# Kernel tuning notes

Measured on AMD Instinct MI355X. Metric: run time of the kernel, lower is better.

Reference implementation:

```python
import jax, jax.numpy as jnp
import numpy as np

T_SYN = 201
SYN_BASIS_NO = 3


def setup_inputs() -> dict:
    key = jax.random.key(0)
    ks = jax.random.split(key, 5)
    T_data, n_e, n_i, sub_no, B = 100000, 500, 200, 20, SYN_BASIS_NO
    S_e = jax.random.uniform(ks[0], (T_data, n_e), jnp.float32)
    S_i = jax.random.uniform(ks[1], (T_data, n_i), jnp.float32)
    C_syn_e = jax.random.uniform(ks[2], (sub_no, n_e), jnp.float32)
    C_syn_i = jax.random.uniform(ks[3], (sub_no, n_i), jnp.float32)
    # init values from the torch module
    K_syn = jnp.concatenate([jnp.full((sub_no, B, 1), 0.02, jnp.float32),
                             jnp.full((sub_no, B, 1), -0.02, jnp.float32)], axis=-1)
    tau_syn = jnp.tile(jnp.arange(1.6, 1.6 + B, dtype=jnp.float32).reshape(-1, 1), (1, 2))
    delta_syn = 2.0 * jax.random.uniform(ks[4], (sub_no, 2), jnp.float32)
    return dict(S_e=S_e, S_i=S_i, C_syn_e=C_syn_e, C_syn_i=C_syn_i,
                K_syn=K_syn, tau_syn=tau_syn, delta_syn=delta_syn)


def _kernels(K_syn, tau_syn, delta_syn):
    # Vectorized alpha-function kernel bank: [sub_no, 2(e/i), T_syn]
    t = jnp.arange(T_SYN, dtype=jnp.float32)                     # [T]
    ts = t[None, None, :] - delta_syn[:, :, None]                # [S,2,T]
    ts = jnp.where(ts < 0.0, 0.0, ts)                            # clamp like t[t<0]=0
    tau = jnp.exp(tau_syn)                                       # [B,2]
    tt = ts[:, None, :, :] / tau[None, :, :, None]               # [S,B,2,T]
    basis = tt * jnp.exp(-tt)                                    # alpha functions
    return jnp.einsum('sbct,sbc->sct', basis, K_syn)             # [S,2,T]


def _causal_conv(x, kern):
    # x: [T_data, S]; kern: [S, T_syn]; out[t,s] = sum_k kern[s,k] * x[t-k,s]
    S = x.shape[1]
    lhs = x.T[None]                          # [1,S,T_data]
    rhs = kern[:, ::-1][:, None, :]          # flip -> lax correlation == causal conv
    out = jax.lax.conv_general_dilated(lhs, rhs, (1,), [(T_SYN - 1, 0)],
                                       feature_group_count=S,
                                       dimension_numbers=('NCH', 'OIH', 'NCH'))
    return out[0].T                          # [T_data, S]


def reference(S_e, S_i, C_syn_e, C_syn_i, K_syn, tau_syn, delta_syn):
    kern = _kernels(K_syn, tau_syn, delta_syn)   # [S,2,T_syn]
    in_e = S_e @ C_syn_e.T                       # [T_data, sub_no]
    in_i = S_i @ C_syn_i.T                       # [T_data, sub_no]
    return _causal_conv(in_e, kern[:, 0]) + _causal_conv(in_i, kern[:, 1])
```

## Files before the change

kernel.cpp:

```cpp
#include <hip/hip_runtime.h>
#include <hip/hip_bf16.h>

#define TDATA 100000
#define NE 500
#define NI 200
#define SUB 20
#define NB 3
#define TSYN 201

#define SROW 100552
#define HROW 216
#define STEPS_E 32
#define STEPS_I 13
#define FULL_E 31
#define FULL_I 12
#define GEMM_BLKS 782

#define OFF_HP  0
#define OFF_BE  8640
#define OFF_BI  (OFF_BE + 8192)
#define OFF_INT (OFF_BI + 3328)

typedef __bf16 bf16x8 __attribute__((ext_vector_type(8)));
typedef float  f32x16 __attribute__((ext_vector_type(16)));

__global__ __launch_bounds__(256) void setup_kernel(
    const float* __restrict__ C_e, const float* __restrict__ C_i,
    const float* __restrict__ K_syn, const float* __restrict__ tau_syn,
    const float* __restrict__ delta_syn, float* __restrict__ ws)
{
    int idx = blockIdx.x * 256 + threadIdx.x;
    if (idx < 8640) {
        int c = idx / (SUB * HROW);
        int rem = idx - c * (SUB * HROW);
        int s = rem / HROW;
        int k = (rem - s * HROW) - 8;
        float v = 0.f;
        if (k >= 0 && k < TSYN) {
            float ts = (float)k - delta_syn[s * 2 + c];
            ts = ts < 0.f ? 0.f : ts;
            #pragma unroll
            for (int b = 0; b < NB; b++) {
                float tt = ts / expf(tau_syn[b * 2 + c]);
                v += K_syn[(s * NB + b) * 2 + c] * tt * expf(-tt);
            }
        }
        ws[OFF_HP + idx] = v;
    } else if (idx < 30720) {
        int j = idx - 8640;
        const int PERROW = 552;
        int row = j / PERROW;
        int e = j - row * PERROW;
        int off = (e < 200) ? e : (200 + TDATA + (e - 200));
        ws[OFF_INT + (long)row * SROW + off] = 0.f;
    } else if (idx < 47104) {
        int j = idx - 30720;
        int step = j >> 9;
        int lane = (j >> 3) & 63;
        int jj = j & 7;
        int k = step * 16 + ((lane >> 5) << 3) + jj;
        int s = lane & 31;
        float v = (s < SUB && k < NE) ? C_e[s * NE + k] : 0.f;
        ((__hip_bfloat16*)(ws + OFF_BE))[j] = (__hip_bfloat16)v;
    } else {
        int j = idx - 47104;
        int step = j >> 9;
        int lane = (j >> 3) & 63;
        int jj = j & 7;
        int k = step * 16 + ((lane >> 5) << 3) + jj;
        int s = lane & 31;
        float v = (s < SUB && k < NI) ? C_i[s * NI + k] : 0.f;
        ((__hip_bfloat16*)(ws + OFF_BI))[j] = (__hip_bfloat16)v;
    }
}

template<int K, int FULL>
__device__ __forceinline__ void gemm_body(
    const float* __restrict__ S, const float* __restrict__ wsA,
    float* __restrict__ inT, long row0, int lane)
{
    const int n = lane & 31, h = lane >> 5;
    long row = row0 + n; if (row >= TDATA) row = TDATA - 1;
    const float* rp = S + row * (long)K + h * 8;
    const bf16x8* afr = (const bf16x8*)wsA;
    f32x16 acc = {};

    #pragma unroll 4
    for (int u = 0; u < FULL; u++) {
        float4 lo = *(const float4*)(rp + 16 * u);
        float4 hi = *(const float4*)(rp + 16 * u + 4);
        bf16x8 b;
        b[0] = (__bf16)lo.x; b[1] = (__bf16)lo.y; b[2] = (__bf16)lo.z; b[3] = (__bf16)lo.w;
        b[4] = (__bf16)hi.x; b[5] = (__bf16)hi.y; b[6] = (__bf16)hi.z; b[7] = (__bf16)hi.w;
        bf16x8 a = afr[u * 64 + lane];
        acc = __builtin_amdgcn_mfma_f32_32x32x16_bf16(a, b, acc, 0, 0, 0);
    }
    {
        int kb = FULL * 16 + h * 8;
        float4 lo = make_float4(0.f, 0.f, 0.f, 0.f);
        float4 hi = make_float4(0.f, 0.f, 0.f, 0.f);
        if (kb + 8 <= K) {
            lo = *(const float4*)(rp + 16 * FULL);
            hi = *(const float4*)(rp + 16 * FULL + 4);
        } else if (kb + 4 <= K) {
            lo = *(const float4*)(rp + 16 * FULL);
        }
        bf16x8 b;
        b[0] = (__bf16)lo.x; b[1] = (__bf16)lo.y; b[2] = (__bf16)lo.z; b[3] = (__bf16)lo.w;
        b[4] = (__bf16)hi.x; b[5] = (__bf16)hi.y; b[6] = (__bf16)hi.z; b[7] = (__bf16)hi.w;
        bf16x8 a = afr[FULL * 64 + lane];
        acc = __builtin_amdgcn_mfma_f32_32x32x16_bf16(a, b, acc, 0, 0, 0);
    }

    long t = row0 + n;
    #pragma unroll
    for (int r = 0; r < 16; r++) {
        int m = (r & 3) + 8 * (r >> 2) + 4 * h;
        if (m < SUB && t < TDATA)
            inT[(long)m * SROW + 200 + t] = acc[r];
    }
}

__global__ __launch_bounds__(256) void gemm_kernel(
    const float* __restrict__ Se, const float* __restrict__ Si,
    float* __restrict__ ws)
{
    int lane = threadIdx.x & 63, wave = threadIdx.x >> 6;
    if (blockIdx.x < GEMM_BLKS) {
        long row0 = (long)blockIdx.x * 128 + wave * 32;
        gemm_body<NE, FULL_E>(Se, ws + OFF_BE, ws + OFF_INT, row0, lane);
    } else {
        long row0 = (long)(blockIdx.x - GEMM_BLKS) * 128 + wave * 32;
        gemm_body<NI, FULL_I>(Si, ws + OFF_BI,
                              ws + OFF_INT + (long)SUB * SROW, row0, lane);
    }
}

#define SW(i) ((i) + ((i) >> 5))

__global__ __launch_bounds__(256) void conv_kernel(
    const float* __restrict__ ws, float* __restrict__ out)
{
    __shared__ __align__(16) float W[2][2336];
    __shared__ __align__(16) float HT[2][208];
    const int tid = threadIdx.x;
    const int s = blockIdx.y;
    const long t0 = (long)blockIdx.x * 2048;

    for (int i = tid; i < 1128; i += 256) {
        int c = i >= 564;
        int i4 = i - c * 564;
        float4 v = *(const float4*)(ws + OFF_INT + (long)(c * SUB + s) * SROW
                                    + t0 - 8 + 4 * i4);
        int b = 4 * i4;
        int p = SW(b);
        W[c][p] = v.x; W[c][p + 1] = v.y; W[c][p + 2] = v.z; W[c][p + 3] = v.w;
    }
    if (tid < 104) {
        int c = tid >= 52;
        int j4 = (tid - c * 52) * 4;
        *(float4*)&HT[c][j4] =
            *(const float4*)(ws + OFF_HP + (c * SUB + s) * HROW + 8 + j4);
    }
    __syncthreads();

    float acc[8];
    #pragma unroll
    for (int r = 0; r < 8; r++) acc[r] = 0.f;

    #pragma unroll
    for (int c = 0; c < 2; c++) {
        #pragma unroll 2
        for (int g = 0; g < 26; g++) {
            int k0 = g << 3;
            int xb = (tid << 3) + 200 - k0;
            float x[16];
            #pragma unroll
            for (int q = 0; q < 16; q++) x[q] = W[c][SW(xb + q)];
            float h[8];
            *(float4*)&h[0] = *(const float4*)&HT[c][k0];
            *(float4*)&h[4] = *(const float4*)&HT[c][k0 + 4];
            #pragma unroll
            for (int j = 0; j < 8; j++)
                #pragma unroll
                for (int r = 0; r < 8; r++)
                    acc[r] += h[j] * x[8 + r - j];
        }
    }

    #pragma unroll
    for (int r = 0; r < 8; r++) {
        long t = t0 + 8 * tid + r;
        if (t < TDATA) out[t * SUB + s] = acc[r];
    }
}

extern "C" void kernel_launch(void* const* d_in, const int* in_sizes, int n_in,
                              void* d_out, int out_size, void* d_ws, size_t ws_size,
                              hipStream_t stream)
{
    const float* S_e     = (const float*)d_in[0];
    const float* S_i     = (const float*)d_in[1];
    const float* C_e     = (const float*)d_in[2];
    const float* C_i     = (const float*)d_in[3];
    const float* K_syn   = (const float*)d_in[4];
    const float* tau_syn = (const float*)d_in[5];
    const float* delta   = (const float*)d_in[6];
    float* out = (float*)d_out;
    float* ws  = (float*)d_ws;

    hipLaunchKernelGGL(setup_kernel, dim3(210), dim3(256), 0, stream,
                       C_e, C_i, K_syn, tau_syn, delta, ws);
    hipLaunchKernelGGL(gemm_kernel, dim3(2 * GEMM_BLKS), dim3(256), 0, stream,
                       S_e, S_i, ws);
    hipLaunchKernelGGL(conv_kernel, dim3(49, SUB), dim3(256), 0, stream,
                       ws, out);
}
```

Measured before the change: 405.7 us.

## Stage GEMM input tiles in LDS via direct global-to-LDS loads with split-K waves

Each block now copies a contiguous 32-row tile of S into shared memory with global_load_lds, so the global reads are fully coalesced instead of strided per-row float4 loads. The four waves then split the K dimension of the MFMA loop and combine their partial accumulators through LDS before wave 0 writes the result. This replaces poorly coalesced HBM access with one bulk copy, at the cost of 64 KB of LDS per block (lower occupancy), a synchronous wait with no overlap, and extra reduction traffic.

Measured after the change: 400.2 us. Within noise of the previous version (-1.3%).

```diff
diff --git a/kernel.cpp b/kernel.cpp
--- a/kernel.cpp
+++ b/kernel.cpp
@@ -12,9 +12,7 @@
 #define HROW 216
 #define STEPS_E 32
 #define STEPS_I 13
-#define FULL_E 31
-#define FULL_I 12
-#define GEMM_BLKS 782
+#define NTILE 3125
 
 #define OFF_HP  0
 #define OFF_BE  8640
@@ -74,50 +72,72 @@
     }
 }
 
-template<int K, int FULL>
-__device__ __forceinline__ void gemm_body(
+template<int K, int STEPS>
+__device__ __forceinline__ void gemm2_body(
     const float* __restrict__ S, const float* __restrict__ wsA,
-    float* __restrict__ inT, long row0, int lane)
-{
+    float* __restrict__ inT, float* tile, int blk, int tid)
+{
+    const long gb = (long)blk * (32 * K);
+    constexpr int TB = 32 * K * 4;
+    {
+        auto gsrc = (const __attribute__((address_space(1))) char*)(const void*)(S + gb);
+        auto ldst = (__attribute__((address_space(3))) char*)(void*)tile;
+        for (int off = tid * 16; off < TB; off += 4096)
+            __builtin_amdgcn_global_load_lds(gsrc + off, ldst + off, 16, 0, 0);
+    }
+    asm volatile("s_waitcnt vmcnt(0)" ::: "memory");
+    __syncthreads();
+
+    const int lane = tid & 63, wave = tid >> 6;
     const int n = lane & 31, h = lane >> 5;
-    long row = row0 + n; if (row >= TDATA) row = TDATA - 1;
-    const float* rp = S + row * (long)K + h * 8;
+    const float* rp = tile + n * K;
     const bf16x8* afr = (const bf16x8*)wsA;
     f32x16 acc = {};
 
     #pragma unroll 4
-    for (int u = 0; u < FULL; u++) {
-        float4 lo = *(const float4*)(rp + 16 * u);
-        float4 hi = *(const float4*)(rp + 16 * u + 4);
+    for (int u = wave; u < STEPS; u += 4) {
+        const int kb = u * 16 + h * 8;
+        float4 lo = make_float4(0.f, 0.f, 0.f, 0.f);
+        float4 hi = make_float4(0.f, 0.f, 0.f, 0.f);
+        if (kb + 8 <= K) {
+            lo = *(const float4*)(rp + kb);
+            hi = *(const float4*)(rp + kb + 4);
+        } else if (kb + 4 <= K) {
+            lo = *(const float4*)(rp + kb);
+        }
         bf16x8 b;
         b[0] = (__bf16)lo.x; b[1] = (__bf16)lo.y; b[2] = (__bf16)lo.z; b[3] = (__bf16)lo.w;
         b[4] = (__bf16)hi.x; b[5] = (__bf16)hi.y; b[6] = (__bf16)hi.z; b[7] = (__bf16)hi.w;
         bf16x8 a = afr[u * 64 + lane];
         acc = __builtin_amdgcn_mfma_f32_32x32x16_bf16(a, b, acc, 0, 0, 0);
     }
-    {
-        int kb = FULL * 16 + h * 8;
-        float4 lo = make_float4(0.f, 0.f, 0.f, 0.f);
-        float4 hi = make_float4(0.f, 0.f, 0.f, 0.f);
-        if (kb + 8 <= K) {
-            lo = *(const float4*)(rp + 16 * FULL);
-            hi = *(const float4*)(rp + 16 * FULL + 4);
-        } else if (kb + 4 <= K) {
-            lo = *(const float4*)(rp + 16 * FULL);
-        }
-        bf16x8 b;
-        b[0] = (__bf16)lo.x; b[1] = (__bf16)lo.y; b[2] = (__bf16)lo.z; b[3] = (__bf16)lo.w;
-        b[4] = (__bf16)hi.x; b[5] = (__bf16)hi.y; b[6] = (__bf16)hi.z; b[7] = (__bf16)hi.w;
-        bf16x8 a = afr[FULL * 64 + lane];
-        acc = __builtin_amdgcn_mfma_f32_32x32x16_bf16(a, b, acc, 0, 0, 0);
-    }
-
-    long t = row0 + n;
-    #pragma unroll
-    for (int r = 0; r < 16; r++) {
-        int m = (r & 3) + 8 * (r >> 2) + 4 * h;
-        if (m < SUB && t < TDATA)
-            inT[(long)m * SROW + 200 + t] = acc[r];
+
+    __syncthreads();
+    if (wave != 0) {
+        float4* dst = (float4*)(tile + ((wave - 1) * 64 + lane) * 16);
+        dst[0] = make_float4(acc[0],  acc[1],  acc[2],  acc[3]);
+        dst[1] = make_float4(acc[4],  acc[5],  acc[6],  acc[7]);
+        dst[2] = make_float4(acc[8],  acc[9],  acc[10], acc[11]);
+        dst[3] = make_float4(acc[12], acc[13], acc[14], acc[15]);
+    }
+    __syncthreads();
+    if (wave == 0) {
+        #pragma unroll
+        for (int w = 0; w < 3; w++) {
+            const float4* src = (const float4*)(tile + (w * 64 + lane) * 16);
+            float4 p0 = src[0], p1 = src[1], p2 = src[2], p3 = src[3];
+            acc[0]  += p0.x; acc[1]  += p0.y; acc[2]  += p0.z; acc[3]  += p0.w;
+            acc[4]  += p1.x; acc[5]  += p1.y; acc[6]  += p1.z; acc[7]  += p1.w;
+            acc[8]  += p2.x; acc[9]  += p2.y; acc[10] += p2.z; acc[11] += p2.w;
+            acc[12] += p3.x; acc[13] += p3.y; acc[14] += p3.z; acc[15] += p3.w;
+        }
+        const long t = (long)blk * 32 + n;
+        #pragma unroll
+        for (int r = 0; r < 16; r++) {
+            int m = (r & 3) + 8 * (r >> 2) + 4 * h;
+            if (m < SUB)
+                inT[(long)m * SROW + 200 + t] = acc[r];
+        }
     }
 }
 
@@ -125,15 +145,14 @@
     const float* __restrict__ Se, const float* __restrict__ Si,
     float* __restrict__ ws)
 {
-    int lane = threadIdx.x & 63, wave = threadIdx.x >> 6;
-    if (blockIdx.x < GEMM_BLKS) {
-        long row0 = (long)blockIdx.x * 128 + wave * 32;
-        gemm_body<NE, FULL_E>(Se, ws + OFF_BE, ws + OFF_INT, row0, lane);
-    } else {
-        long row0 = (long)(blockIdx.x - GEMM_BLKS) * 128 + wave * 32;
-        gemm_body<NI, FULL_I>(Si, ws + OFF_BI,
-                              ws + OFF_INT + (long)SUB * SROW, row0, lane);
-    }
+    __shared__ float tile[32 * NE];
+    const int tid = threadIdx.x;
+    if (blockIdx.x < NTILE)
+        gemm2_body<NE, STEPS_E>(Se, ws + OFF_BE, ws + OFF_INT,
+                                tile, blockIdx.x, tid);
+    else
+        gemm2_body<NI, STEPS_I>(Si, ws + OFF_BI, ws + OFF_INT + (long)SUB * SROW,
+                                tile, blockIdx.x - NTILE, tid);
 }
 
 #define SW(i) ((i) + ((i) >> 5))
@@ -211,7 +230,7 @@
 
     hipLaunchKernelGGL(setup_kernel, dim3(210), dim3(256), 0, stream,
                        C_e, C_i, K_syn, tau_syn, delta, ws);
-    hipLaunchKernelGGL(gemm_kernel, dim3(2 * GEMM_BLKS), dim3(256), 0, stream,
+    hipLaunchKernelGGL(gemm_kernel, dim3(2 * NTILE), dim3(256), 0, stream,
                        S_e, S_i, ws);
     hipLaunchKernelGGL(conv_kernel, dim3(49, SUB), dim3(256), 0, stream,
                        ws, out);
```

## Stream GEMM input through LDS with async double-buffered loads and reuse conv registers

Applied to the files above, without the earlier changes.

The GEMM now stages S rows into per-wave LDS buffers with global_load_lds, double-buffering 32-column chunks so loads overlap MFMA work. It also preloads the A fragments into registers and uses an XOR swizzle to avoid bank conflicts. The conv kernel switches to vectorized float4 LDS reads with a sliding register window that reuses the previous group's data instead of reloading 16 scalars per group. The aim is to hide global memory latency in the memory-bound GEMM, at the cost of more registers and reliance on manual vmcnt waits. Setup grid and padding sizes change to match the new chunk layout.

After: 1.196 ms. 195% more time.

```diff
diff --git a/kernel.cpp b/kernel.cpp
--- a/kernel.cpp
+++ b/kernel.cpp
@@ -10,16 +10,14 @@
 
 #define SROW 100552
 #define HROW 216
-#define STEPS_E 32
-#define STEPS_I 13
-#define FULL_E 31
-#define FULL_I 12
-#define GEMM_BLKS 782
+#define NC_E 16
+#define NC_I 7
+#define NBLK 782
 
 #define OFF_HP  0
 #define OFF_BE  8640
 #define OFF_BI  (OFF_BE + 8192)
-#define OFF_INT (OFF_BI + 3328)
+#define OFF_INT (OFF_BI + 3584)
 
 typedef __bf16 bf16x8 __attribute__((ext_vector_type(8)));
 typedef float  f32x16 __attribute__((ext_vector_type(16)));
@@ -74,49 +72,78 @@
     }
 }
 
-template<int K, int FULL>
-__device__ __forceinline__ void gemm_body(
+template<int K>
+__device__ __forceinline__ void issue_chunk(
+    const float* __restrict__ S, const float* __restrict__ zrp,
+    long row0, int c, float* buf, int rsel, int slotl)
+{
+    #pragma unroll
+    for (int q = 0; q < 4; q++) {
+        const int kg = c * 32 + slotl;
+        const float* src = (kg + 4 <= K)
+            ? (S + (row0 + 8 * q + rsel) * (long)K + kg) : zrp;
+        __builtin_amdgcn_global_load_lds(
+            (const __attribute__((address_space(1))) char*)(const void*)src,
+            (__attribute__((address_space(3))) char*)(void*)(buf + q * 256),
+            16, 0, 0);
+    }
+}
+
+template<int K, int NC>
+__device__ __forceinline__ void gemm3_body(
     const float* __restrict__ S, const float* __restrict__ wsA,
-    float* __restrict__ inT, long row0, int lane)
-{
+    float* __restrict__ inT, const float* __restrict__ zrp,
+    float* buf0, float* buf1, long tile, int lane)
+{
+    constexpr int NSTEP = 2 * NC;
+    const long row0 = tile * 32;
     const int n = lane & 31, h = lane >> 5;
-    long row = row0 + n; if (row >= TDATA) row = TDATA - 1;
-    const float* rp = S + row * (long)K + h * 8;
+    const int rsel = lane >> 3;
+    const int slotl = 4 * ((lane & 7) ^ rsel);
+    const int xr = (n & 7) << 2;
+
     const bf16x8* afr = (const bf16x8*)wsA;
+    bf16x8 A[NSTEP];
+    #pragma unroll
+    for (int u = 0; u < NSTEP; u++) A[u] = afr[u * 64 + lane];
+
+    issue_chunk<K>(S, zrp, row0, 0, buf0, rsel, slotl);
+    issue_chunk<K>(S, zrp, row0, 1, buf1, rsel, slotl);
+
     f32x16 acc = {};
-
-    #pragma unroll 4
-    for (int u = 0; u < FULL; u++) {
-        float4 lo = *(const float4*)(rp + 16 * u);
-        float4 hi = *(const float4*)(rp + 16 * u + 4);
-        bf16x8 b;
-        b[0] = (__bf16)lo.x; b[1] = (__bf16)lo.y; b[2] = (__bf16)lo.z; b[3] = (__bf16)lo.w;
-        b[4] = (__bf16)hi.x; b[5] = (__bf16)hi.y; b[6] = (__bf16)hi.z; b[7] = (__bf16)hi.w;
-        bf16x8 a = afr[u * 64 + lane];
-        acc = __builtin_amdgcn_mfma_f32_32x32x16_bf16(a, b, acc, 0, 0, 0);
-    }
-    {
-        int kb = FULL * 16 + h * 8;
-        float4 lo = make_float4(0.f, 0.f, 0.f, 0.f);
-        float4 hi = make_float4(0.f, 0.f, 0.f, 0.f);
-        if (kb + 8 <= K) {
-            lo = *(const float4*)(rp + 16 * FULL);
-            hi = *(const float4*)(rp + 16 * FULL + 4);
-        } else if (kb + 4 <= K) {
-            lo = *(const float4*)(rp + 16 * FULL);
+    #pragma unroll
+    for (int c = 0; c < NC; c++) {
+        if (c < NC - 1) asm volatile("s_waitcnt vmcnt(4)" ::: "memory");
+        else            asm volatile("s_waitcnt vmcnt(0)" ::: "memory");
+        __builtin_amdgcn_sched_barrier(0);
+
+        float* buf = (c & 1) ? buf1 : buf0;
+        const float* r0 = buf + n * 32;
+        bf16x8 bf[2];
+        #pragma unroll
+        for (int uu = 0; uu < 2; uu++) {
+            const int kl = 16 * uu + 8 * h;
+            float4 lo = *(const float4*)(r0 + (kl ^ xr));
+            float4 hi = *(const float4*)(r0 + ((kl + 4) ^ xr));
+            bf16x8 b;
+            b[0] = (__bf16)lo.x; b[1] = (__bf16)lo.y; b[2] = (__bf16)lo.z; b[3] = (__bf16)lo.w;
+            b[4] = (__bf16)hi.x; b[5] = (__bf16)hi.y; b[6] = (__bf16)hi.z; b[7] = (__bf16)hi.w;
+            bf[uu] = b;
         }
-        bf16x8 b;
-        b[0] = (__bf16)lo.x; b[1] = (__bf16)lo.y; b[2] = (__bf16)lo.z; b[3] = (__bf16)lo.w;
-        b[4] = (__bf16)hi.x; b[5] = (__bf16)hi.y; b[6] = (__bf16)hi.z; b[7] = (__bf16)hi.w;
-        bf16x8 a = afr[FULL * 64 + lane];
-        acc = __builtin_amdgcn_mfma_f32_32x32x16_bf16(a, b, acc, 0, 0, 0);
-    }
-
-    long t = row0 + n;
+        __builtin_amdgcn_sched_barrier(0);
+        if (c + 2 < NC)
+            issue_chunk<K>(S, zrp, row0, c + 2, buf, rsel, slotl);
+        #pragma unroll
+        for (int uu = 0; uu < 2; uu++)
+            acc = __builtin_amdgcn_mfma_f32_32x32x16_bf16(A[2 * c + uu], bf[uu],
+                                                          acc, 0, 0, 0);
+    }
+
+    const long t = row0 + n;
     #pragma unroll
     for (int r = 0; r < 16; r++) {
         int m = (r & 3) + 8 * (r >> 2) + 4 * h;
-        if (m < SUB && t < TDATA)
+        if (m < SUB)
             inT[(long)m * SROW + 200 + t] = acc[r];
     }
 }
@@ -125,66 +152,83 @@
     const float* __restrict__ Se, const float* __restrict__ Si,
     float* __restrict__ ws)
 {
-    int lane = threadIdx.x & 63, wave = threadIdx.x >> 6;
-    if (blockIdx.x < GEMM_BLKS) {
-        long row0 = (long)blockIdx.x * 128 + wave * 32;
-        gemm_body<NE, FULL_E>(Se, ws + OFF_BE, ws + OFF_INT, row0, lane);
+    __shared__ float lds[4][2][1024];
+    const int lane = threadIdx.x & 63, wave = threadIdx.x >> 6;
+    if (blockIdx.x < NBLK) {
+        long tile = (long)blockIdx.x * 4 + wave;
+        if (tile >= 3125) return;
+        gemm3_body<NE, NC_E>(Se, ws + OFF_BE, ws + OFF_INT, ws + OFF_INT,
+                             lds[wave][0], lds[wave][1], tile, lane);
     } else {
-        long row0 = (long)(blockIdx.x - GEMM_BLKS) * 128 + wave * 32;
-        gemm_body<NI, FULL_I>(Si, ws + OFF_BI,
-                              ws + OFF_INT + (long)SUB * SROW, row0, lane);
-    }
-}
-
-#define SW(i) ((i) + ((i) >> 5))
+        long tile = (long)(blockIdx.x - NBLK) * 4 + wave;
+        if (tile >= 3125) return;
+        gemm3_body<NI, NC_I>(Si, ws + OFF_BI, ws + OFF_INT + (long)SUB * SROW,
+                             ws + OFF_INT, lds[wave][0], lds[wave][1], tile, lane);
+    }
+}
+
+#define SW(i) ((i) + (((i) >> 5) << 2))
+
+#define CONV_G(G, LO, HI, DOLOAD) {                                        \
+    float4 h0 = *(const float4*)&HT[c][8 * (G)];                           \
+    float4 h1 = *(const float4*)&HT[c][8 * (G) + 4];                       \
+    float hv[8] = {h0.x, h0.y, h0.z, h0.w, h1.x, h1.y, h1.z, h1.w};        \
+    _Pragma("unroll")                                                      \
+    for (int j = 0; j < 8; j++) {                                          \
+        _Pragma("unroll")                                                  \
+        for (int r = 0; r < 8; r++) {                                      \
+            const int ix = 8 + r - j;                                      \
+            acc[r] += hv[j] * ((ix < 8) ? LO[ix] : HI[ix - 8]);            \
+        }                                                                  \
+    }                                                                      \
+    if (DOLOAD) {                                                          \
+        const int a0 = wb + 216 - 8 * (G);                                 \
+        *(float4*)&LO[0] = *(const float4*)&W[c][SW(a0)];                  \
+        *(float4*)&LO[4] = *(const float4*)&W[c][SW(a0 + 4)];              \
+    }                                                                      \
+}
 
 __global__ __launch_bounds__(256) void conv_kernel(
     const float* __restrict__ ws, float* __restrict__ out)
 {
-    __shared__ __align__(16) float W[2][2336];
+    __shared__ __align__(16) float W[2][2560];
     __shared__ __align__(16) float HT[2][208];
     const int tid = threadIdx.x;
     const int s = blockIdx.y;
     const long t0 = (long)blockIdx.x * 2048;
 
     for (int i = tid; i < 1128; i += 256) {
-        int c = i >= 564;
-        int i4 = i - c * 564;
-        float4 v = *(const float4*)(ws + OFF_INT + (long)(c * SUB + s) * SROW
+        int cch = i >= 564;
+        int i4 = i - cch * 564;
+        float4 v = *(const float4*)(ws + OFF_INT + (long)(cch * SUB + s) * SROW
                                     + t0 - 8 + 4 * i4);
-        int b = 4 * i4;
-        int p = SW(b);
-        W[c][p] = v.x; W[c][p + 1] = v.y; W[c][p + 2] = v.z; W[c][p + 3] = v.w;
+        *(float4*)&W[cch][SW(4 * i4)] = v;
     }
     if (tid < 104) {
-        int c = tid >= 52;
-        int j4 = (tid - c * 52) * 4;
-        *(float4*)&HT[c][j4] =
-            *(const float4*)(ws + OFF_HP + (c * SUB + s) * HROW + 8 + j4);
+        int cch = tid >= 52;
+        int j4 = (tid - cch * 52) * 4;
+        *(float4*)&HT[cch][j4] =
+            *(const float4*)(ws + OFF_HP + (cch * SUB + s) * HROW + 8 + j4);
     }
     __syncthreads();
 
     float acc[8];
     #pragma unroll
     for (int r = 0; r < 8; r++) acc[r] = 0.f;
+    const int wb = tid << 3;
 
     #pragma unroll
     for (int c = 0; c < 2; c++) {
-        #pragma unroll 2
-        for (int g = 0; g < 26; g++) {
-            int k0 = g << 3;
-            int xb = (tid << 3) + 200 - k0;
-            float x[16];
-            #pragma unroll
-            for (int q = 0; q < 16; q++) x[q] = W[c][SW(xb + q)];
-            float h[8];
-            *(float4*)&h[0] = *(const float4*)&HT[c][k0];
-            *(float4*)&h[4] = *(const float4*)&HT[c][k0 + 4];
-            #pragma unroll
-            for (int j = 0; j < 8; j++)
-                #pragma unroll
-                for (int r = 0; r < 8; r++)
-                    acc[r] += h[j] * x[8 + r - j];
+        float xa[8], xb2[8];
+        *(float4*)&xa[0]  = *(const float4*)&W[c][SW(wb)];
+        *(float4*)&xa[4]  = *(const float4*)&W[c][SW(wb + 4)];
+        *(float4*)&xb2[0] = *(const float4*)&W[c][SW(wb + 8)];
+        *(float4*)&xb2[4] = *(const float4*)&W[c][SW(wb + 12)];
+        #pragma unroll
+        for (int gg = 0; gg < 13; gg++) {
+            const int g1 = 25 - 2 * gg, g0 = g1 - 1;
+            CONV_G(g1, xa, xb2, 1);
+            CONV_G(g0, xb2, xa, (g0 != 0));
         }
     }
 
@@ -209,9 +253,9 @@
     float* out = (float*)d_out;
     float* ws  = (float*)d_ws;
 
-    hipLaunchKernelGGL(setup_kernel, dim3(210), dim3(256), 0, stream,
+    hipLaunchKernelGGL(setup_kernel, dim3(212), dim3(256), 0, stream,
                        C_e, C_i, K_syn, tau_syn, delta, ws);
-    hipLaunchKernelGGL(gemm_kernel, dim3(2 * GEMM_BLKS), dim3(256), 0, stream,
+    hipLaunchKernelGGL(gemm_kernel, dim3(2 * NBLK), dim3(256), 0, stream,
                        S_e, S_i, ws);
     hipLaunchKernelGGL(conv_kernel, dim3(49, SUB), dim3(256), 0, stream,
                        ws, out);
```
